# Kernel tuning notes

Measured on AMD Instinct MI355X. Metric: run time of the kernel, lower is better.

The kernel has to match this reference:

```python
import jax, jax.numpy as jnp
import numpy as np

CMD, LIDAR, H, T = 2, 360, 256, 50
B = 2048


def _cell(x, h, c, Wih, Whh, b):
    # PyTorch LSTM: gates ordered (i, f, g, o)
    g = x @ Wih.T + h @ Whh.T + b
    i, f, gg, o = jnp.split(g, 4, axis=-1)
    c = jax.nn.sigmoid(f) * c + jax.nn.sigmoid(i) * jnp.tanh(gg)
    h = jax.nn.sigmoid(o) * jnp.tanh(c)
    return h, c


def setup_inputs() -> dict:
    key = jax.random.key(0)
    ks = jax.random.split(key, 10)
    s = 0.05  # small init so tanh/sigmoid stay in sane range
    return {
        "past_data": jax.random.normal(ks[0], (B, T, CMD + LIDAR), jnp.float32),
        "future_cmds": jax.random.normal(ks[1], (B, T, CMD), jnp.float32),
        "enc_Wih": jax.random.normal(ks[2], (4 * H, CMD + LIDAR), jnp.float32) * s,
        "enc_Whh": jax.random.normal(ks[3], (4 * H, H), jnp.float32) * s,
        "enc_b": jax.random.normal(ks[4], (4 * H,), jnp.float32) * s,
        "dec_Wih": jax.random.normal(ks[5], (4 * H, LIDAR + CMD), jnp.float32) * s,
        "dec_Whh": jax.random.normal(ks[6], (4 * H, H), jnp.float32) * s,
        "dec_b": jax.random.normal(ks[7], (4 * H,), jnp.float32) * s,
        "out_W": jax.random.normal(ks[8], (LIDAR, H), jnp.float32) * s,
        "out_b": jax.random.normal(ks[9], (LIDAR,), jnp.float32) * s,
    }


def reference(past_data, future_cmds, enc_Wih, enc_Whh, enc_b,
              dec_Wih, dec_Whh, dec_b, out_W, out_b):
    b = past_data.shape[0]
    h0 = jnp.zeros((b, H), past_data.dtype)
    c0 = jnp.zeros((b, H), past_data.dtype)

    # ---- encoder LSTM over past_data ----
    def enc_step(carry, x):
        h, c = carry
        h, c = _cell(x, h, c, enc_Wih, enc_Whh, enc_b)
        return (h, c), None

    (h, c), _ = jax.lax.scan(enc_step, (h0, c0), jnp.swapaxes(past_data, 0, 1))

    lidar0 = past_data[:, -1, CMD:]  # [B, LIDAR]

    def dec_step(carry, cmd):
        h, c, lidar = carry
        x = jnp.concatenate([lidar, cmd], axis=-1)  # [B, LIDAR+CMD]
        h, c = _cell(x, h, c, dec_Wih, dec_Whh, dec_b)
        lidar = h @ out_W.T + out_b
        return (h, c, lidar), lidar

    _, preds = jax.lax.scan(dec_step, (h, c, lidar0), jnp.swapaxes(future_cmds, 0, 1))
    return jnp.swapaxes(preds, 0, 1)  # [B, T, LIDAR]
```

## Files before the change

### kernel.cpp

```cpp
#include <hip/hip_runtime.h>
#include <hip/hip_bf16.h>
#include <math.h>

#define CMDN   2
#define LIDARN 360
#define HN     256
#define TN     50
#define BATCH  2048
#define KXN    362
#define NG     1024
#define KP     384
#define MR     (TN*BATCH)
#define SLAB   ((size_t)BATCH*HN)
#define NOF    24

typedef __attribute__((ext_vector_type(8))) short bf16x8;
typedef __attribute__((ext_vector_type(4))) float f32x4;

__device__ inline unsigned short f2b(float f) {
    unsigned int x = __builtin_bit_cast(unsigned int, f);
    x += 0x7FFFu + ((x >> 16) & 1u);
    return (unsigned short)(x >> 16);
}
__device__ inline float b2f(unsigned short u) {
    unsigned int x = ((unsigned int)u) << 16;
    return __builtin_bit_cast(float, x);
}
__device__ inline float sigf(float x)  { return 1.f / (1.f + __expf(-x)); }
__device__ inline float tanhfa(float x){ return 2.f / (1.f + __expf(-2.f * x)) - 1.f; }

__device__ inline int p2j(int p) { return ((p & 3) << 8) + (p >> 2); }

typedef const __attribute__((address_space(1))) unsigned int* gp1_t;
typedef __attribute__((address_space(3))) unsigned int* lp3_t;
__device__ inline void gload16(const void* g, void* l) {
    __builtin_amdgcn_global_load_lds((gp1_t)g, (lp3_t)l, 16, 0, 0);
}

__global__ __launch_bounds__(256) void pack_xb(
    const float* __restrict__ past, unsigned short* __restrict__ Xb)
{
    int c = blockIdx.x * 256 + threadIdx.x;
    if (c >= MR * (KP / 8)) return;
    int r = c / (KP / 8), kc = c - r * (KP / 8);
    int b = r & 2047, t = r >> 11;
    const float* p = past + ((size_t)b * TN + t) * KXN;
    const int k = kc * 8;
    bf16x8 v;
    if (k + 8 <= KXN) {
        float2 f0 = *(const float2*)(p + k);
        float2 f1 = *(const float2*)(p + k + 2);
        float2 f2 = *(const float2*)(p + k + 4);
        float2 f3 = *(const float2*)(p + k + 6);
        v[0] = (short)f2b(f0.x); v[1] = (short)f2b(f0.y);
        v[2] = (short)f2b(f1.x); v[3] = (short)f2b(f1.y);
        v[4] = (short)f2b(f2.x); v[5] = (short)f2b(f2.y);
        v[6] = (short)f2b(f3.x); v[7] = (short)f2b(f3.y);
    } else {
        #pragma unroll
        for (int e = 0; e < 8; ++e)
            v[e] = (k + e < KXN) ? (short)f2b(p[k + e]) : (short)0;
    }
    *(bf16x8*)&Xb[(size_t)r * KP + k] = v;
}

template<int OMODE>
__global__ __launch_bounds__(256) void gemm_fast(
    const unsigned short* __restrict__ A,
    const unsigned short* __restrict__ B,
    const float* __restrict__ bias,
    void* __restrict__ Cv, int K, int ldc)
{
    __shared__ __align__(16) unsigned short As[128 * 32];
    __shared__ __align__(16) unsigned short Bs[128 * 32];

    const int nwg = gridDim.x * gridDim.y;
    const int hid = blockIdx.y * gridDim.x + blockIdx.x;
    const int lid = (hid & 7) * (nwg >> 3) + (hid >> 3);
    const int bx  = lid % gridDim.x;
    const int by  = lid / gridDim.x;

    const int tid  = threadIdx.x;
    const int lane = tid & 63;
    const int wv   = tid >> 6;
    const int wm   = wv >> 1, wn = wv & 1;
    const int r0   = by * 128;
    const int n0   = bx * 128;
    const int l15  = lane & 15;
    const int lhi  = lane >> 4;

    const int srow = lane >> 2;
    const int sc   = lane & 3;

    f32x4 acc[4][4] = {};

    for (int k0 = 0; k0 < K; k0 += 32) {
        #pragma unroll
        for (int j = 0; j < 2; ++j) {
            const int rl = (wv * 2 + j) * 16 + srow;
            const int cs = sc ^ (rl & 3);
            gload16(&A[(size_t)(r0 + rl) * K + k0 + cs * 8], &As[(wv * 2 + j) * 512]);
            gload16(&B[(size_t)(n0 + rl) * K + k0 + cs * 8], &Bs[(wv * 2 + j) * 512]);
        }
        __syncthreads();
        bf16x8 a[4], b[4];
        #pragma unroll
        for (int i = 0; i < 4; ++i) {
            const int ra = wm * 64 + i * 16 + l15;
            const int rb = wn * 64 + i * 16 + l15;
            a[i] = *(const bf16x8*)&As[ra * 32 + (lhi ^ (ra & 3)) * 8];
            b[i] = *(const bf16x8*)&Bs[rb * 32 + (lhi ^ (rb & 3)) * 8];
        }
        #pragma unroll
        for (int mi = 0; mi < 4; ++mi)
            #pragma unroll
            for (int ni = 0; ni < 4; ++ni)
                acc[mi][ni] = __builtin_amdgcn_mfma_f32_16x16x32_bf16(a[mi], b[ni], acc[mi][ni], 0, 0, 0);
        __syncthreads();
    }

    #pragma unroll
    for (int mi = 0; mi < 4; ++mi) {
        const int rowb = r0 + wm * 64 + mi * 16 + ((lane >> 4) << 2);
        #pragma unroll
        for (int ni = 0; ni < 4; ++ni) {
            const int col = n0 + wn * 64 + ni * 16 + l15;
            #pragma unroll
            for (int r = 0; r < 4; ++r) {
                const int row = rowb + r;
                float v = acc[mi][ni][r];
                if (OMODE == 0) {
                    ((float*)Cv)[(size_t)row * ldc + col] = v + bias[col];
                } else if (OMODE == 2) {
                    ((unsigned short*)Cv)[(size_t)row * ldc + col] = f2b(v + bias[col]);
                } else {
                    if (col < LIDARN)
                        ((float*)Cv)[(size_t)row * (TN * LIDARN) + (size_t)(TN - 1) * LIDARN + col]
                            = v + bias[col];
                }
            }
        }
    }
}

template<int MODE>
__global__ __launch_bounds__(512, 4) void step5(
    const unsigned short* __restrict__ hsrc,
    const unsigned short* __restrict__ Wf,
    const unsigned short* __restrict__ addb,
    const float* __restrict__ biasf,
    const float* __restrict__ cmdw,
    const float* __restrict__ cmds_t,
    const unsigned short* __restrict__ oWf,
    const float* __restrict__ ob,
    float* __restrict__ out,
    int tprev,
    float* __restrict__ ct,
    unsigned short* __restrict__ hdst)
{
    __shared__ __align__(16) unsigned short Hl[32 * 264];
    __shared__ __align__(16) unsigned short Xl[32 * 128];
    __shared__ float cmdl[32][2];

    const int tid  = threadIdx.x;
    const int lane = tid & 63;
    const int w    = tid >> 6;
    const int l15  = lane & 15;
    const int lhi  = lane >> 4;
    const int g    = l15 & 3;
    const int cg   = blockIdx.x >> 6;
    const int rg   = blockIdx.x & 63;
    const int r0   = rg * 32;

    const unsigned short* wb = Wf + (size_t)(cg * 8 + w) * 4096;
    bf16x8 breg[8];
    #pragma unroll
    for (int kf = 0; kf < 8; ++kf)
        breg[kf] = *(const bf16x8*)&wb[(size_t)(kf * 64 + lane) * 8];

    #pragma unroll
    for (int i = 0; i < 2; ++i) {
        const int c = i * 512 + tid;
        const int row = c >> 5, col8 = c & 31;
        *(bf16x8*)&Hl[row * 264 + col8 * 8] =
            *(const bf16x8*)&hsrc[(size_t)(r0 + row) * HN + col8 * 8];
    }
    if (MODE <= 1) {
        const unsigned short* xs = addb + (size_t)r0 * NG + cg * 128;
        const int row = tid >> 4, col8 = tid & 15;
        *(bf16x8*)&Xl[row * 128 + col8 * 8] =
            *(const bf16x8*)&xs[(size_t)row * NG + col8 * 8];
    }
    if (MODE >= 1 && tid < 32) {
        const float2 cv = *(const float2*)&cmds_t[(size_t)(r0 + tid) * (TN * CMDN)];
        cmdl[tid][0] = cv.x; cmdl[tid][1] = cv.y;
    }
    __syncthreads();

    f32x4 acc[2] = {};
    #pragma unroll
    for (int kf = 0; kf < 8; ++kf) {
        #pragma unroll
        for (int mf = 0; mf < 2; ++mf) {
            bf16x8 a = *(const bf16x8*)&Hl[(mf * 16 + l15) * 264 + kf * 32 + lhi * 8];
            acc[mf] = __builtin_amdgcn_mfma_f32_16x16x32_bf16(a, breg[kf], acc[mf], 0, 0, 0);
        }
    }

    f32x4 acc_o = {};
    const int s_o = w & 1;
    const int f_o = w >> 1;
    if (MODE == 2 && f_o < 3) {
        const int fg = cg * 3 + f_o;
        #pragma unroll
        for (int kf = 0; kf < 8; ++kf) {
            bf16x8 a = *(const bf16x8*)&Hl[(s_o * 16 + l15) * 264 + kf * 32 + lhi * 8];
            bf16x8 b = *(const bf16x8*)&oWf[(size_t)((fg * 8 + kf) * 64 + lane) * 8];
            acc_o = __builtin_amdgcn_mfma_f32_16x16x32_bf16(a, b, acc_o, 0, 0, 0);
        }
    }

    const int p = cg * 128 + w * 16 + l15;
    const int u = cg * 32 + w * 4 + (l15 >> 2);
    float w0_r = 0.f, w1_r = 0.f, bf_r = 0.f;
    if (MODE >= 1) { w0_r = cmdw[p * 2]; w1_r = cmdw[p * 2 + 1]; }
    if (MODE == 2) bf_r = biasf[p];
    #pragma unroll
    for (int mf = 0; mf < 2; ++mf) {
        float* cp = (g == 0) ? &ct[(size_t)u * BATCH + r0 + mf * 16 + lhi * 4] : nullptr;
        f32x4 c4 = (g == 0) ? *(const f32x4*)cp : f32x4{0.f, 0.f, 0.f, 0.f};
        #pragma unroll
        for (int r = 0; r < 4; ++r) {
            const int rw = mf * 16 + lhi * 4 + r;
            float v = acc[mf][r];
            if (MODE <= 1) v += b2f(Xl[rw * 128 + w * 16 + l15]);
            if (MODE == 2) v += bf_r;
            if (MODE >= 1) v += cmdl[rw][0] * w0_r + cmdl[rw][1] * w1_r;
            float act = (g == 2) ? tanhfa(v) : sigf(v);
            float a1 = __shfl_xor(act, 1);
            float a2 = __shfl_xor(act, 2);
            float a3 = __shfl_xor(act, 3);
            if (g == 0) {
                float cc = a1 * c4[r] + act * a2;
                c4[r] = cc;
                hdst[(size_t)(r0 + rw) * HN + u] = f2b(a3 * tanhfa(cc));
            }
        }
        if (g == 0) *(f32x4*)cp = c4;
    }

    if (MODE == 2 && f_o < 3) {
        const int col = (cg * 3 + f_o) * 16 + l15;
        if (col < LIDARN) {
            const float bo = ob[col];
            #pragma unroll
            for (int r = 0; r < 4; ++r) {
                const int brow = r0 + s_o * 16 + lhi * 4 + r;
                out[(size_t)brow * (TN * LIDARN) + (size_t)tprev * LIDARN + col]
                    = acc_o[r] + bo;
            }
        }
    }
}

__global__ __launch_bounds__(256) void pack_w(
    const float* __restrict__ past,
    const float* __restrict__ eWih, const float* __restrict__ eb,
    const float* __restrict__ dWih, const float* __restrict__ db,
    const float* __restrict__ oW,   const float* __restrict__ ob,
    unsigned short* __restrict__ L0b,
    unsigned short* __restrict__ Wihe_p,
    unsigned short* __restrict__ Wdihl_p,
    unsigned short* __restrict__ oWp,
    unsigned short* __restrict__ oWf,
    float* __restrict__ Wc_p,
    float* __restrict__ ebp, float* __restrict__ dbp,
    float* __restrict__ biasf,
    unsigned short* __restrict__ h0, float* __restrict__ ct)
{
    int idx = blockIdx.x * 256 + threadIdx.x;
    if (idx < BATCH * KP) {
        int b = idx / KP, k = idx - b * KP;
        L0b[idx] = (k < LIDARN)
            ? f2b(past[((size_t)b * TN + (TN - 1)) * KXN + CMDN + k]) : (unsigned short)0;
    }
    if (idx < NG * KP) {
        int p = idx / KP, k = idx - p * KP;
        int j = p2j(p);
        Wihe_p[idx]  = (k < KXN)    ? f2b(eWih[(size_t)j * KXN + k]) : (unsigned short)0;
        Wdihl_p[idx] = (k < LIDARN) ? f2b(dWih[(size_t)j * KXN + k]) : (unsigned short)0;
        if (k < 2) Wc_p[p * 2 + k] = dWih[(size_t)j * KXN + LIDARN + k];
        if (k == 0) { ebp[p] = eb[j]; dbp[p] = db[j]; }
    }
    if (idx < KP * HN) {
        int n = idx / HN, k = idx - n * HN;
        oWp[idx] = (n < LIDARN) ? f2b(oW[(size_t)n * HN + k]) : (unsigned short)0;
    }
    if (idx < NOF * 8 * 64 * 8) {
        int e = idx & 7, lane = (idx >> 3) & 63, kf = (idx >> 9) & 7, f = idx >> 12;
        int n = f * 16 + (lane & 15);
        int k = kf * 32 + (lane >> 4) * 8 + e;
        oWf[idx] = (n < LIDARN) ? f2b(oW[(size_t)n * HN + k]) : (unsigned short)0;
    }
    if (idx < BATCH * HN) { h0[idx] = 0; ct[idx] = 0.f; }
    if (idx < NG) {
        int j = p2j(idx);
        float s = db[j];
        for (int n = 0; n < LIDARN; ++n)
            s += dWih[(size_t)j * KXN + n] * ob[n];
        biasf[idx] = s;
    }
}

__global__ __launch_bounds__(256) void wcomb_kernel(
    const float* __restrict__ dWih, const float* __restrict__ dWhh,
    const float* __restrict__ oW, float* __restrict__ Wcomb_f)
{
    const int pb = blockIdx.x * 4, k = threadIdx.x;
    int j0 = p2j(pb), j1 = p2j(pb + 1), j2 = p2j(pb + 2), j3 = p2j(pb + 3);
    float s0 = dWhh[(size_t)j0 * HN + k];
    float s1 = dWhh[(size_t)j1 * HN + k];
    float s2 = dWhh[(size_t)j2 * HN + k];
    float s3 = dWhh[(size_t)j3 * HN + k];
    #pragma unroll 4
    for (int n = 0; n < LIDARN; ++n) {
        const float ow = oW[(size_t)n * HN + k];
        s0 += dWih[(size_t)j0 * KXN + n] * ow;
        s1 += dWih[(size_t)j1 * KXN + n] * ow;
        s2 += dWih[(size_t)j2 * KXN + n] * ow;
        s3 += dWih[(size_t)j3 * KXN + n] * ow;
    }
    Wcomb_f[(size_t)pb * HN + k]            = s0;
    Wcomb_f[(size_t)(pb + 1) * HN + k]      = s1;
    Wcomb_f[(size_t)(pb + 2) * HN + k]      = s2;
    Wcomb_f[(size_t)(pb + 3) * HN + k]      = s3;
}

__global__ __launch_bounds__(256) void pack_wfrag(
    const float* __restrict__ eWhh, const float* __restrict__ dWhh,
    const float* __restrict__ Wcomb_f,
    unsigned short* __restrict__ Wf_enc,
    unsigned short* __restrict__ Wf_dec0,
    unsigned short* __restrict__ Wf_dec)
{
    const int NW = NG * HN;
    int idx = blockIdx.x * 256 + threadIdx.x;
    if (idx >= 3 * NW) return;
    int sel = idx / NW;
    int d   = idx - sel * NW;
    int e    = d & 7;
    int lane = (d >> 3) & 63;
    int kf   = (d >> 9) & 7;
    int cf   = d >> 12;
    int p = cf * 16 + (lane & 15);
    int k = kf * 32 + (lane >> 4) * 8 + e;
    if (sel == 0)      Wf_enc[d]  = f2b(eWhh[(size_t)p2j(p) * HN + k]);
    else if (sel == 1) Wf_dec0[d] = f2b(dWhh[(size_t)p2j(p) * HN + k]);
    else               Wf_dec[d]  = f2b(Wcomb_f[(size_t)p * HN + k]);
}

extern "C" void kernel_launch(void* const* d_in, const int* in_sizes, int n_in,
                              void* d_out, int out_size, void* d_ws, size_t ws_size,
                              hipStream_t stream)
{
    const float* past = (const float*)d_in[0];
    const float* cmds = (const float*)d_in[1];
    const float* eWih = (const float*)d_in[2];
    const float* eWhh = (const float*)d_in[3];
    const float* eb   = (const float*)d_in[4];
    const float* dWih = (const float*)d_in[5];
    const float* dWhh = (const float*)d_in[6];
    const float* db   = (const float*)d_in[7];
    const float* oW   = (const float*)d_in[8];
    const float* ob   = (const float*)d_in[9];
    float* out = (float*)d_out;

    char* w = (char*)d_ws;
    auto alloc = [&](size_t bytes) {
        char* p = w; w += (bytes + 255) & ~(size_t)255; return p;
    };
    unsigned short* xw      = (unsigned short*)alloc((size_t)MR * NG * 2);
    unsigned short* Xb      = (unsigned short*)alloc((size_t)MR * KP * 2);
    unsigned short* hdec    = (unsigned short*)alloc((size_t)MR * HN * 2);
    unsigned short* l0wb    = (unsigned short*)alloc((size_t)BATCH * NG * 2);
    unsigned short* hpp     = (unsigned short*)alloc(2 * SLAB * 2);
    float*          ct      = (float*)alloc(SLAB * 4);
    float*          Wcomb_f = (float*)alloc((size_t)NG * HN * 4);
    unsigned short* Wf_enc  = (unsigned short*)alloc((size_t)NG * HN * 2);
    unsigned short* Wf_dec0 = (unsigned short*)alloc((size_t)NG * HN * 2);
    unsigned short* Wf_dec  = (unsigned short*)alloc((size_t)NG * HN * 2);
    unsigned short* oWf     = (unsigned short*)alloc((size_t)NOF * 8 * 64 * 8 * 2);
    unsigned short* L0b     = (unsigned short*)alloc((size_t)BATCH * KP * 2);
    unsigned short* Wihe_p  = (unsigned short*)alloc((size_t)NG * KP * 2);
    unsigned short* Wdihl_p = (unsigned short*)alloc((size_t)NG * KP * 2);
    unsigned short* oWp     = (unsigned short*)alloc((size_t)KP * HN * 2);
    float*          Wc_p    = (float*)alloc((size_t)NG * 2 * 4);
    float*          ebp     = (float*)alloc(NG * 4);
    float*          dbp     = (float*)alloc(NG * 4);
    float*          biasf   = (float*)alloc(NG * 4);

    pack_w<<<(BATCH * KP + 255) / 256, 256, 0, stream>>>(
        past, eWih, eb, dWih, db, oW, ob,
        L0b, Wihe_p, Wdihl_p, oWp, oWf, Wc_p, ebp, dbp, biasf, hpp, ct);
    wcomb_kernel<<<NG / 4, 256, 0, stream>>>(dWih, dWhh, oW, Wcomb_f);
    pack_wfrag<<<(3 * NG * HN + 255) / 256, 256, 0, stream>>>(
        eWhh, dWhh, Wcomb_f, Wf_enc, Wf_dec0, Wf_dec);
    pack_xb<<<(MR * (KP / 8) + 255) / 256, 256, 0, stream>>>(past, Xb);

    gemm_fast<2><<<dim3(NG / 128, MR / 128), 256, 0, stream>>>(
        Xb, Wihe_p, ebp, xw, KP, NG);
    gemm_fast<2><<<dim3(NG / 128, BATCH / 128), 256, 0, stream>>>(
        L0b, Wdihl_p, dbp, l0wb, KP, NG);

    for (int t = 0; t < TN; ++t) {
        const unsigned short* hs = hpp + (size_t)(t & 1) * SLAB;
        unsigned short*       hd = hpp + (size_t)((t + 1) & 1) * SLAB;
        step5<0><<<512, 512, 0, stream>>>(
            hs, Wf_enc, xw + (size_t)t * BATCH * NG,
            nullptr, nullptr, nullptr, nullptr, nullptr, nullptr, 0, ct, hd);
    }
    step5<1><<<512, 512, 0, stream>>>(
        hpp + (size_t)(TN & 1) * SLAB, Wf_dec0, l0wb,
        nullptr, Wc_p, cmds, nullptr, nullptr, nullptr, 0, ct, hdec);
    for (int t = 1; t < TN; ++t) {
        step5<2><<<512, 512, 0, stream>>>(
            hdec + (size_t)(t - 1) * SLAB, Wf_dec, nullptr,
            biasf, Wc_p, cmds + (size_t)t * CMDN,
            oWf, ob, out, t - 1, ct, hdec + (size_t)t * SLAB);
    }
    gemm_fast<3><<<dim3(KP / 128, BATCH / 128), 256, 0, stream>>>(
        hdec + (size_t)(TN - 1) * SLAB, oWp, ob, out, HN, 0);
}
```

Before: 1.137 ms.

## Fuse all 100 LSTM recurrence steps into one persistent kernel

Replaces the 100 per-timestep step5 launches and the final output GEMM with a single persistent kernel. Each block owns 16 batch rows for the whole sequence, keeps c in registers and h double-buffered in LDS, and prefetches the next step's input projection with nontemporal loads. The per-step output projection and its store are also done inside the kernel. This removes launch overhead and the global round-trips for h and c. In exchange, only 128 blocks of 1024 threads run, and each step re-streams the recurrent weights from global/L2 instead of holding them in registers, so parallelism drops and weight traffic may rise.

```diff
diff --git a/kernel.cpp b/kernel.cpp
--- a/kernel.cpp
+++ b/kernel.cpp
@@ -11,11 +11,11 @@
 #define NG     1024
 #define KP     384
 #define MR     (TN*BATCH)
-#define SLAB   ((size_t)BATCH*HN)
 #define NOF    24
 
 typedef __attribute__((ext_vector_type(8))) short bf16x8;
 typedef __attribute__((ext_vector_type(4))) float f32x4;
+typedef __attribute__((ext_vector_type(4))) unsigned int u32x4;
 
 __device__ inline unsigned short f2b(float f) {
     unsigned int x = __builtin_bit_cast(unsigned int, f);
@@ -28,6 +28,11 @@
 }
 __device__ inline float sigf(float x)  { return 1.f / (1.f + __expf(-x)); }
 __device__ inline float tanhfa(float x){ return 2.f / (1.f + __expf(-2.f * x)) - 1.f; }
+
+__device__ inline bf16x8 ntload8(const unsigned short* p) {
+    u32x4 v = __builtin_nontemporal_load((const u32x4*)p);
+    return __builtin_bit_cast(bf16x8, v);
+}
 
 __device__ inline int p2j(int p) { return ((p & 3) << 8) + (p >> 2); }
 
@@ -64,12 +69,11 @@
     *(bf16x8*)&Xb[(size_t)r * KP + k] = v;
 }
 
-template<int OMODE>
 __global__ __launch_bounds__(256) void gemm_fast(
     const unsigned short* __restrict__ A,
     const unsigned short* __restrict__ B,
     const float* __restrict__ bias,
-    void* __restrict__ Cv, int K, int ldc)
+    unsigned short* __restrict__ C, int K, int ldc)
 {
     __shared__ __align__(16) unsigned short As[128 * 32];
     __shared__ __align__(16) unsigned short Bs[128 * 32];
@@ -126,41 +130,28 @@
         for (int ni = 0; ni < 4; ++ni) {
             const int col = n0 + wn * 64 + ni * 16 + l15;
             #pragma unroll
-            for (int r = 0; r < 4; ++r) {
-                const int row = rowb + r;
-                float v = acc[mi][ni][r];
-                if (OMODE == 0) {
-                    ((float*)Cv)[(size_t)row * ldc + col] = v + bias[col];
-                } else if (OMODE == 2) {
-                    ((unsigned short*)Cv)[(size_t)row * ldc + col] = f2b(v + bias[col]);
-                } else {
-                    if (col < LIDARN)
-                        ((float*)Cv)[(size_t)row * (TN * LIDARN) + (size_t)(TN - 1) * LIDARN + col]
-                            = v + bias[col];
-                }
-            }
-        }
-    }
-}
-
-template<int MODE>
-__global__ __launch_bounds__(512, 4) void step5(
-    const unsigned short* __restrict__ hsrc,
-    const unsigned short* __restrict__ Wf,
-    const unsigned short* __restrict__ addb,
+            for (int r = 0; r < 4; ++r)
+                C[(size_t)(rowb + r) * ldc + col] = f2b(acc[mi][ni][r] + bias[col]);
+        }
+    }
+}
+
+__global__ __launch_bounds__(1024, 4) void recur_fused(
+    const unsigned short* __restrict__ xw,
+    const unsigned short* __restrict__ l0wb,
     const float* __restrict__ biasf,
     const float* __restrict__ cmdw,
-    const float* __restrict__ cmds_t,
+    const float* __restrict__ cmds,
+    const unsigned short* __restrict__ Wf_enc,
+    const unsigned short* __restrict__ Wf_dec0,
+    const unsigned short* __restrict__ Wf_dec,
     const unsigned short* __restrict__ oWf,
-    const float* __restrict__ ob,
-    float* __restrict__ out,
-    int tprev,
-    float* __restrict__ ct,
-    unsigned short* __restrict__ hdst)
-{
-    __shared__ __align__(16) unsigned short Hl[32 * 264];
-    __shared__ __align__(16) unsigned short Xl[32 * 128];
-    __shared__ float cmdl[32][2];
+    const float* __restrict__ obias,
+    float* __restrict__ out)
+{
+    __shared__ __align__(16) unsigned short Hl[2][16][264];
+    __shared__ __align__(16) unsigned short Xl[2][16384];
+    __shared__ float cmdl[TN][16][2];
 
     const int tid  = threadIdx.x;
     const int lane = tid & 63;
@@ -168,96 +159,117 @@
     const int l15  = lane & 15;
     const int lhi  = lane >> 4;
     const int g    = l15 & 3;
-    const int cg   = blockIdx.x >> 6;
-    const int rg   = blockIdx.x & 63;
-    const int r0   = rg * 32;
-
-    const unsigned short* wb = Wf + (size_t)(cg * 8 + w) * 4096;
-    bf16x8 breg[8];
+    const int r0   = blockIdx.x * 16;
+
+    float w0c[4], w1c[4], bfv[4];
     #pragma unroll
-    for (int kf = 0; kf < 8; ++kf)
-        breg[kf] = *(const bf16x8*)&wb[(size_t)(kf * 64 + lane) * 8];
-
-    #pragma unroll
-    for (int i = 0; i < 2; ++i) {
-        const int c = i * 512 + tid;
-        const int row = c >> 5, col8 = c & 31;
-        *(bf16x8*)&Hl[row * 264 + col8 * 8] =
-            *(const bf16x8*)&hsrc[(size_t)(r0 + row) * HN + col8 * 8];
-    }
-    if (MODE <= 1) {
-        const unsigned short* xs = addb + (size_t)r0 * NG + cg * 128;
-        const int row = tid >> 4, col8 = tid & 15;
-        *(bf16x8*)&Xl[row * 128 + col8 * 8] =
-            *(const bf16x8*)&xs[(size_t)row * NG + col8 * 8];
-    }
-    if (MODE >= 1 && tid < 32) {
-        const float2 cv = *(const float2*)&cmds_t[(size_t)(r0 + tid) * (TN * CMDN)];
-        cmdl[tid][0] = cv.x; cmdl[tid][1] = cv.y;
+    for (int ni = 0; ni < 4; ++ni) {
+        const int p = w * 64 + ni * 16 + l15;
+        w0c[ni] = cmdw[p * 2];
+        w1c[ni] = cmdw[p * 2 + 1];
+        bfv[ni] = biasf[p];
+    }
+
+    if (tid < 528) {
+        const bf16x8 z = {0, 0, 0, 0, 0, 0, 0, 0};
+        ((bf16x8*)&Hl[0][0][0])[tid] = z;
+    }
+    if (tid < 800) {
+        const int rr = tid / TN, t = tid - rr * TN;
+        const float2 cv = *(const float2*)&cmds[(size_t)(r0 + rr) * (TN * CMDN) + t * CMDN];
+        cmdl[t][rr][0] = cv.x; cmdl[t][rr][1] = cv.y;
+    }
+    {
+        const unsigned short* s0 = xw + (size_t)r0 * NG;
+        ((bf16x8*)Xl[1])[tid]        = *(const bf16x8*)&s0[(size_t)tid * 8];
+        ((bf16x8*)Xl[1])[tid + 1024] = *(const bf16x8*)&s0[(size_t)(tid + 1024) * 8];
     }
     __syncthreads();
 
-    f32x4 acc[2] = {};
-    #pragma unroll
-    for (int kf = 0; kf < 8; ++kf) {
-        #pragma unroll
-        for (int mf = 0; mf < 2; ++mf) {
-            bf16x8 a = *(const bf16x8*)&Hl[(mf * 16 + l15) * 264 + kf * 32 + lhi * 8];
-            acc[mf] = __builtin_amdgcn_mfma_f32_16x16x32_bf16(a, breg[kf], acc[mf], 0, 0, 0);
-        }
-    }
-
-    f32x4 acc_o = {};
-    const int s_o = w & 1;
-    const int f_o = w >> 1;
-    if (MODE == 2 && f_o < 3) {
-        const int fg = cg * 3 + f_o;
+    float c_reg[4][4] = {};
+
+    for (int s = 1; s <= 100; ++s) {
+        const unsigned short* src =
+            (s <= 49) ? xw + ((size_t)s * BATCH + r0) * NG :
+            (s == 50) ? l0wb + (size_t)r0 * NG : nullptr;
+        bf16x8 pf0, pf1;
+        if (src) {
+            pf0 = ntload8(&src[(size_t)tid * 8]);
+            pf1 = ntload8(&src[(size_t)(tid + 1024) * 8]);
+        }
+
+        const unsigned short* Wb = (s <= 50) ? Wf_enc : (s == 51) ? Wf_dec0 : Wf_dec;
+        const int ib = (s - 1) & 1, obuf = s & 1;
+
+        f32x4 acc[4] = {};
         #pragma unroll
         for (int kf = 0; kf < 8; ++kf) {
-            bf16x8 a = *(const bf16x8*)&Hl[(s_o * 16 + l15) * 264 + kf * 32 + lhi * 8];
-            bf16x8 b = *(const bf16x8*)&oWf[(size_t)((fg * 8 + kf) * 64 + lane) * 8];
-            acc_o = __builtin_amdgcn_mfma_f32_16x16x32_bf16(a, b, acc_o, 0, 0, 0);
-        }
-    }
-
-    const int p = cg * 128 + w * 16 + l15;
-    const int u = cg * 32 + w * 4 + (l15 >> 2);
-    float w0_r = 0.f, w1_r = 0.f, bf_r = 0.f;
-    if (MODE >= 1) { w0_r = cmdw[p * 2]; w1_r = cmdw[p * 2 + 1]; }
-    if (MODE == 2) bf_r = biasf[p];
-    #pragma unroll
-    for (int mf = 0; mf < 2; ++mf) {
-        float* cp = (g == 0) ? &ct[(size_t)u * BATCH + r0 + mf * 16 + lhi * 4] : nullptr;
-        f32x4 c4 = (g == 0) ? *(const f32x4*)cp : f32x4{0.f, 0.f, 0.f, 0.f};
-        #pragma unroll
-        for (int r = 0; r < 4; ++r) {
-            const int rw = mf * 16 + lhi * 4 + r;
-            float v = acc[mf][r];
-            if (MODE <= 1) v += b2f(Xl[rw * 128 + w * 16 + l15]);
-            if (MODE == 2) v += bf_r;
-            if (MODE >= 1) v += cmdl[rw][0] * w0_r + cmdl[rw][1] * w1_r;
-            float act = (g == 2) ? tanhfa(v) : sigf(v);
-            float a1 = __shfl_xor(act, 1);
-            float a2 = __shfl_xor(act, 2);
-            float a3 = __shfl_xor(act, 3);
-            if (g == 0) {
-                float cc = a1 * c4[r] + act * a2;
-                c4[r] = cc;
-                hdst[(size_t)(r0 + rw) * HN + u] = f2b(a3 * tanhfa(cc));
+            bf16x8 a = *(const bf16x8*)&Hl[ib][l15][kf * 32 + lhi * 8];
+            #pragma unroll
+            for (int ni = 0; ni < 4; ++ni) {
+                bf16x8 b = *(const bf16x8*)&Wb[(size_t)(((w * 4 + ni) * 8 + kf) * 64 + lane) * 8];
+                acc[ni] = __builtin_amdgcn_mfma_f32_16x16x32_bf16(a, b, acc[ni], 0, 0, 0);
             }
         }
-        if (g == 0) *(f32x4*)cp = c4;
-    }
-
-    if (MODE == 2 && f_o < 3) {
-        const int col = (cg * 3 + f_o) * 16 + l15;
-        if (col < LIDARN) {
-            const float bo = ob[col];
+
+        if (src) {
+            ((bf16x8*)Xl[(s + 1) & 1])[tid]        = pf0;
+            ((bf16x8*)Xl[(s + 1) & 1])[tid + 1024] = pf1;
+        }
+
+        const int tdec = (s >= 51) ? s - 51 : 0;
+        #pragma unroll
+        for (int ni = 0; ni < 4; ++ni) {
+            const int p = w * 64 + ni * 16 + l15;
             #pragma unroll
             for (int r = 0; r < 4; ++r) {
-                const int brow = r0 + s_o * 16 + lhi * 4 + r;
-                out[(size_t)brow * (TN * LIDARN) + (size_t)tprev * LIDARN + col]
-                    = acc_o[r] + bo;
+                const int rw = lhi * 4 + r;
+                float v = acc[ni][r];
+                if (s <= 51) v += b2f(Xl[s & 1][rw * 1024 + p]);
+                if (s >= 52) v += bfv[ni];
+                if (s >= 51) v += cmdl[tdec][rw][0] * w0c[ni] + cmdl[tdec][rw][1] * w1c[ni];
+                float act = (g == 2) ? tanhfa(v) : sigf(v);
+                float a1 = __shfl_xor(act, 1);
+                float a2 = __shfl_xor(act, 2);
+                float a3 = __shfl_xor(act, 3);
+                if (g == 0) {
+                    float cc = a1 * c_reg[ni][r] + act * a2;
+                    c_reg[ni][r] = cc;
+                    Hl[obuf][rw][w * 16 + ni * 4 + (l15 >> 2)] = f2b(a3 * tanhfa(cc));
+                }
+            }
+        }
+        __syncthreads();
+
+        if (s >= 51) {
+            const int nf = (w < 8) ? 2 : 1;
+            const int f0 = (w < 8) ? w * 2 : (w + 8);
+            f32x4 acc_o[2] = {};
+            #pragma unroll
+            for (int kf = 0; kf < 8; ++kf) {
+                bf16x8 a = *(const bf16x8*)&Hl[obuf][l15][kf * 32 + lhi * 8];
+                #pragma unroll
+                for (int i = 0; i < 2; ++i) {
+                    if (i < nf) {
+                        bf16x8 b = *(const bf16x8*)&oWf[(size_t)(((f0 + i) * 8 + kf) * 64 + lane) * 8];
+                        acc_o[i] = __builtin_amdgcn_mfma_f32_16x16x32_bf16(a, b, acc_o[i], 0, 0, 0);
+                    }
+                }
+            }
+            #pragma unroll
+            for (int i = 0; i < 2; ++i) {
+                if (i < nf) {
+                    const int col = (f0 + i) * 16 + l15;
+                    if (col < LIDARN) {
+                        const float bo = obias[col];
+                        #pragma unroll
+                        for (int r = 0; r < 4; ++r) {
+                            const int rw = lhi * 4 + r;
+                            __builtin_nontemporal_store(acc_o[i][r] + bo,
+                                &out[(size_t)(r0 + rw) * (TN * LIDARN) + (size_t)tdec * LIDARN + col]);
+                        }
+                    }
+                }
             }
         }
     }
@@ -271,12 +283,10 @@
     unsigned short* __restrict__ L0b,
     unsigned short* __restrict__ Wihe_p,
     unsigned short* __restrict__ Wdihl_p,
-    unsigned short* __restrict__ oWp,
     unsigned short* __restrict__ oWf,
     float* __restrict__ Wc_p,
     float* __restrict__ ebp, float* __restrict__ dbp,
-    float* __restrict__ biasf,
-    unsigned short* __restrict__ h0, float* __restrict__ ct)
+    float* __restrict__ biasf)
 {
     int idx = blockIdx.x * 256 + threadIdx.x;
     if (idx < BATCH * KP) {
@@ -292,17 +302,12 @@
         if (k < 2) Wc_p[p * 2 + k] = dWih[(size_t)j * KXN + LIDARN + k];
         if (k == 0) { ebp[p] = eb[j]; dbp[p] = db[j]; }
     }
-    if (idx < KP * HN) {
-        int n = idx / HN, k = idx - n * HN;
-        oWp[idx] = (n < LIDARN) ? f2b(oW[(size_t)n * HN + k]) : (unsigned short)0;
-    }
     if (idx < NOF * 8 * 64 * 8) {
         int e = idx & 7, lane = (idx >> 3) & 63, kf = (idx >> 9) & 7, f = idx >> 12;
         int n = f * 16 + (lane & 15);
         int k = kf * 32 + (lane >> 4) * 8 + e;
         oWf[idx] = (n < LIDARN) ? f2b(oW[(size_t)n * HN + k]) : (unsigned short)0;
     }
-    if (idx < BATCH * HN) { h0[idx] = 0; ct[idx] = 0.f; }
     if (idx < NG) {
         int j = p2j(idx);
         float s = db[j];
@@ -330,10 +335,10 @@
         s2 += dWih[(size_t)j2 * KXN + n] * ow;
         s3 += dWih[(size_t)j3 * KXN + n] * ow;
     }
-    Wcomb_f[(size_t)pb * HN + k]            = s0;
-    Wcomb_f[(size_t)(pb + 1) * HN + k]      = s1;
-    Wcomb_f[(size_t)(pb + 2) * HN + k]      = s2;
-    Wcomb_f[(size_t)(pb + 3) * HN + k]      = s3;
+    Wcomb_f[(size_t)pb * HN + k]       = s0;
+    Wcomb_f[(size_t)(pb + 1) * HN + k] = s1;
+    Wcomb_f[(size_t)(pb + 2) * HN + k] = s2;
+    Wcomb_f[(size_t)(pb + 3) * HN + k] = s3;
 }
 
 __global__ __launch_bounds__(256) void pack_wfrag(
@@ -381,10 +386,7 @@
     };
     unsigned short* xw      = (unsigned short*)alloc((size_t)MR * NG * 2);
     unsigned short* Xb      = (unsigned short*)alloc((size_t)MR * KP * 2);
-    unsigned short* hdec    = (unsigned short*)alloc((size_t)MR * HN * 2);
     unsigned short* l0wb    = (unsigned short*)alloc((size_t)BATCH * NG * 2);
-    unsigned short* hpp     = (unsigned short*)alloc(2 * SLAB * 2);
-    float*          ct      = (float*)alloc(SLAB * 4);
     float*          Wcomb_f = (float*)alloc((size_t)NG * HN * 4);
     unsigned short* Wf_enc  = (unsigned short*)alloc((size_t)NG * HN * 2);
     unsigned short* Wf_dec0 = (unsigned short*)alloc((size_t)NG * HN * 2);
@@ -393,7 +395,6 @@
     unsigned short* L0b     = (unsigned short*)alloc((size_t)BATCH * KP * 2);
     unsigned short* Wihe_p  = (unsigned short*)alloc((size_t)NG * KP * 2);
     unsigned short* Wdihl_p = (unsigned short*)alloc((size_t)NG * KP * 2);
-    unsigned short* oWp     = (unsigned short*)alloc((size_t)KP * HN * 2);
     float*          Wc_p    = (float*)alloc((size_t)NG * 2 * 4);
     float*          ebp     = (float*)alloc(NG * 4);
     float*          dbp     = (float*)alloc(NG * 4);
@@ -401,33 +402,17 @@
 
     pack_w<<<(BATCH * KP + 255) / 256, 256, 0, stream>>>(
         past, eWih, eb, dWih, db, oW, ob,
-        L0b, Wihe_p, Wdihl_p, oWp, oWf, Wc_p, ebp, dbp, biasf, hpp, ct);
+        L0b, Wihe_p, Wdihl_p, oWf, Wc_p, ebp, dbp, biasf);
     wcomb_kernel<<<NG / 4, 256, 0, stream>>>(dWih, dWhh, oW, Wcomb_f);
     pack_wfrag<<<(3 * NG * HN + 255) / 256, 256, 0, stream>>>(
         eWhh, dWhh, Wcomb_f, Wf_enc, Wf_dec0, Wf_dec);
     pack_xb<<<(MR * (KP / 8) + 255) / 256, 256, 0, stream>>>(past, Xb);
 
-    gemm_fast<2><<<dim3(NG / 128, MR / 128), 256, 0, stream>>>(
+    gemm_fast<<<dim3(NG / 128, MR / 128), 256, 0, stream>>>(
         Xb, Wihe_p, ebp, xw, KP, NG);
-    gemm_fast<2><<<dim3(NG / 128, BATCH / 128), 256, 0, stream>>>(
+    gemm_fast<<<dim3(NG / 128, BATCH / 128), 256, 0, stream>>>(
         L0b, Wdihl_p, dbp, l0wb, KP, NG);
 
-    for (int t = 0; t < TN; ++t) {
-        const unsigned short* hs = hpp + (size_t)(t & 1) * SLAB;
-        unsigned short*       hd = hpp + (size_t)((t + 1) & 1) * SLAB;
-        step5<0><<<512, 512, 0, stream>>>(
-            hs, Wf_enc, xw + (size_t)t * BATCH * NG,
-            nullptr, nullptr, nullptr, nullptr, nullptr, nullptr, 0, ct, hd);
-    }
-    step5<1><<<512, 512, 0, stream>>>(
-        hpp + (size_t)(TN & 1) * SLAB, Wf_dec0, l0wb,
-        nullptr, Wc_p, cmds, nullptr, nullptr, nullptr, 0, ct, hdec);
-    for (int t = 1; t < TN; ++t) {
-        step5<2><<<512, 512, 0, stream>>>(
-            hdec + (size_t)(t - 1) * SLAB, Wf_dec, nullptr,
-            biasf, Wc_p, cmds + (size_t)t * CMDN,
-            oWf, ob, out, t - 1, ct, hdec + (size_t)t * SLAB);
-    }
-    gemm_fast<3><<<dim3(KP / 128, BATCH / 128), 256, 0, stream>>>(
-        hdec + (size_t)(TN - 1) * SLAB, oWp, ob, out, HN, 0);
-}
+    recur_fused<<<BATCH / 16, 1024, 0, stream>>>(
+        xw, l0wb, biasf, Wc_p, cmds, Wf_enc, Wf_dec0, Wf_dec, oWf, ob, out);
+}
```

Measured after the change: 1.486 ms. 30.7% more time.

## Deepen GEMM K-tile to 64 and stream recurrent weights inside step loop

Applied to the files above, without the earlier changes.

The input-projection GEMM now stages 64-wide K slices with an 8-way XOR swizzle, which halves the number of barrier pairs per K loop in exchange for twice the LDS per block. The recurrent step kernel no longer preloads all eight weight fragments into registers before the hidden-state staging. It loads each fragment just before its MFMA, cutting register pressure but putting global loads on the MFMA critical path. The unused fp32 output mode of the GEMM is removed.

```diff
diff --git a/kernel.cpp b/kernel.cpp
--- a/kernel.cpp
+++ b/kernel.cpp
@@ -16,6 +16,7 @@
 
 typedef __attribute__((ext_vector_type(8))) short bf16x8;
 typedef __attribute__((ext_vector_type(4))) float f32x4;
+typedef __attribute__((ext_vector_type(4))) unsigned int u32x4;
 
 __device__ inline unsigned short f2b(float f) {
     unsigned int x = __builtin_bit_cast(unsigned int, f);
@@ -71,8 +72,8 @@
     const float* __restrict__ bias,
     void* __restrict__ Cv, int K, int ldc)
 {
-    __shared__ __align__(16) unsigned short As[128 * 32];
-    __shared__ __align__(16) unsigned short Bs[128 * 32];
+    __shared__ __align__(16) unsigned short As[128 * 64];
+    __shared__ __align__(16) unsigned short Bs[128 * 64];
 
     const int nwg = gridDim.x * gridDim.y;
     const int hid = blockIdx.y * gridDim.x + blockIdx.x;
@@ -89,39 +90,42 @@
     const int l15  = lane & 15;
     const int lhi  = lane >> 4;
 
-    const int srow = lane >> 2;
-    const int sc   = lane & 3;
+    const int srow8 = lane >> 3;
+    const int sp    = lane & 7;
 
     f32x4 acc[4][4] = {};
 
-    for (int k0 = 0; k0 < K; k0 += 32) {
-        #pragma unroll
-        for (int j = 0; j < 2; ++j) {
-            const int rl = (wv * 2 + j) * 16 + srow;
-            const int cs = sc ^ (rl & 3);
-            gload16(&A[(size_t)(r0 + rl) * K + k0 + cs * 8], &As[(wv * 2 + j) * 512]);
-            gload16(&B[(size_t)(n0 + rl) * K + k0 + cs * 8], &Bs[(wv * 2 + j) * 512]);
+    for (int k0 = 0; k0 < K; k0 += 64) {
+        #pragma unroll
+        for (int j = 0; j < 4; ++j) {
+            const int rl = (wv * 4 + j) * 8 + srow8;
+            const int cs = sp ^ (rl & 7);
+            gload16(&A[(size_t)(r0 + rl) * K + k0 + cs * 8], &As[(wv * 4 + j) * 512]);
+            gload16(&B[(size_t)(n0 + rl) * K + k0 + cs * 8], &Bs[(wv * 4 + j) * 512]);
         }
         __syncthreads();
-        bf16x8 a[4], b[4];
-        #pragma unroll
-        for (int i = 0; i < 4; ++i) {
-            const int ra = wm * 64 + i * 16 + l15;
-            const int rb = wn * 64 + i * 16 + l15;
-            a[i] = *(const bf16x8*)&As[ra * 32 + (lhi ^ (ra & 3)) * 8];
-            b[i] = *(const bf16x8*)&Bs[rb * 32 + (lhi ^ (rb & 3)) * 8];
-        }
-        #pragma unroll
-        for (int mi = 0; mi < 4; ++mi)
+        #pragma unroll
+        for (int kh = 0; kh < 2; ++kh) {
+            bf16x8 a[4], b[4];
             #pragma unroll
-            for (int ni = 0; ni < 4; ++ni)
-                acc[mi][ni] = __builtin_amdgcn_mfma_f32_16x16x32_bf16(a[mi], b[ni], acc[mi][ni], 0, 0, 0);
+            for (int i = 0; i < 4; ++i) {
+                const int ra = wm * 64 + i * 16 + l15;
+                const int rb = wn * 64 + i * 16 + l15;
+                a[i] = *(const bf16x8*)&As[ra * 64 + (((kh * 4 + lhi) ^ (ra & 7)) * 8)];
+                b[i] = *(const bf16x8*)&Bs[rb * 64 + (((kh * 4 + lhi) ^ (rb & 7)) * 8)];
+            }
+            #pragma unroll
+            for (int mi = 0; mi < 4; ++mi)
+                #pragma unroll
+                for (int ni = 0; ni < 4; ++ni)
+                    acc[mi][ni] = __builtin_amdgcn_mfma_f32_16x16x32_bf16(a[mi], b[ni], acc[mi][ni], 0, 0, 0);
+        }
         __syncthreads();
     }
 
     #pragma unroll
     for (int mi = 0; mi < 4; ++mi) {
-        const int rowb = r0 + wm * 64 + mi * 16 + ((lane >> 4) << 2);
+        const int rowb = r0 + wm * 64 + mi * 16 + (lhi << 2);
         #pragma unroll
         for (int ni = 0; ni < 4; ++ni) {
             const int col = n0 + wn * 64 + ni * 16 + l15;
@@ -129,9 +133,7 @@
             for (int r = 0; r < 4; ++r) {
                 const int row = rowb + r;
                 float v = acc[mi][ni][r];
-                if (OMODE == 0) {
-                    ((float*)Cv)[(size_t)row * ldc + col] = v + bias[col];
-                } else if (OMODE == 2) {
+                if (OMODE == 2) {
                     ((unsigned short*)Cv)[(size_t)row * ldc + col] = f2b(v + bias[col]);
                 } else {
                     if (col < LIDARN)
@@ -144,7 +146,7 @@
 }
 
 template<int MODE>
-__global__ __launch_bounds__(512, 4) void step5(
+__global__ __launch_bounds__(512, 4) void step4(
     const unsigned short* __restrict__ hsrc,
     const unsigned short* __restrict__ Wf,
     const unsigned short* __restrict__ addb,
@@ -172,12 +174,6 @@
     const int rg   = blockIdx.x & 63;
     const int r0   = rg * 32;
 
-    const unsigned short* wb = Wf + (size_t)(cg * 8 + w) * 4096;
-    bf16x8 breg[8];
-    #pragma unroll
-    for (int kf = 0; kf < 8; ++kf)
-        breg[kf] = *(const bf16x8*)&wb[(size_t)(kf * 64 + lane) * 8];
-
     #pragma unroll
     for (int i = 0; i < 2; ++i) {
         const int c = i * 512 + tid;
@@ -197,13 +193,15 @@
     }
     __syncthreads();
 
+    const unsigned short* wb = Wf + (size_t)(cg * 8 + w) * 4096;
     f32x4 acc[2] = {};
     #pragma unroll
     for (int kf = 0; kf < 8; ++kf) {
+        bf16x8 b = *(const bf16x8*)&wb[(size_t)(kf * 64 + lane) * 8];
         #pragma unroll
         for (int mf = 0; mf < 2; ++mf) {
             bf16x8 a = *(const bf16x8*)&Hl[(mf * 16 + l15) * 264 + kf * 32 + lhi * 8];
-            acc[mf] = __builtin_amdgcn_mfma_f32_16x16x32_bf16(a, breg[kf], acc[mf], 0, 0, 0);
+            acc[mf] = __builtin_amdgcn_mfma_f32_16x16x32_bf16(a, b, acc[mf], 0, 0, 0);
         }
     }
 
@@ -330,10 +328,10 @@
         s2 += dWih[(size_t)j2 * KXN + n] * ow;
         s3 += dWih[(size_t)j3 * KXN + n] * ow;
     }
-    Wcomb_f[(size_t)pb * HN + k]            = s0;
-    Wcomb_f[(size_t)(pb + 1) * HN + k]      = s1;
-    Wcomb_f[(size_t)(pb + 2) * HN + k]      = s2;
-    Wcomb_f[(size_t)(pb + 3) * HN + k]      = s3;
+    Wcomb_f[(size_t)pb * HN + k]       = s0;
+    Wcomb_f[(size_t)(pb + 1) * HN + k] = s1;
+    Wcomb_f[(size_t)(pb + 2) * HN + k] = s2;
+    Wcomb_f[(size_t)(pb + 3) * HN + k] = s3;
 }
 
 __global__ __launch_bounds__(256) void pack_wfrag(
@@ -415,15 +413,15 @@
     for (int t = 0; t < TN; ++t) {
         const unsigned short* hs = hpp + (size_t)(t & 1) * SLAB;
         unsigned short*       hd = hpp + (size_t)((t + 1) & 1) * SLAB;
-        step5<0><<<512, 512, 0, stream>>>(
+        step4<0><<<512, 512, 0, stream>>>(
             hs, Wf_enc, xw + (size_t)t * BATCH * NG,
             nullptr, nullptr, nullptr, nullptr, nullptr, nullptr, 0, ct, hd);
     }
-    step5<1><<<512, 512, 0, stream>>>(
+    step4<1><<<512, 512, 0, stream>>>(
         hpp + (size_t)(TN & 1) * SLAB, Wf_dec0, l0wb,
         nullptr, Wc_p, cmds, nullptr, nullptr, nullptr, 0, ct, hdec);
     for (int t = 1; t < TN; ++t) {
-        step5<2><<<512, 512, 0, stream>>>(
+        step4<2><<<512, 512, 0, stream>>>(
             hdec + (size_t)(t - 1) * SLAB, Wf_dec, nullptr,
             biasf, Wc_p, cmds + (size_t)t * CMDN,
             oWf, ob, out, t - 1, ct, hdec + (size_t)t * SLAB);
```

Measured after the change: 1.137 ms. No clear change (+0.0%).
